# Performance work log

Hardware: AMD Instinct MI355X
Metric: run time of the kernel (lower is better)

## Reference

```python
import jax, jax.numpy as jnp
import numpy as np

N, E = 50000, 800000
IN_DIM, HID, HEADS, OUT_DIM, EDGE_DIM = 128, 32, 4, 64, 32


def _glorot(key, shape, dtype=jnp.float32):
    fan_in, fan_out = shape[0], shape[1]
    lim = np.sqrt(6.0 / (fan_in + fan_out))
    return jax.random.uniform(key, shape, dtype, -lim, lim)


def setup_inputs() -> dict:
    key = jax.random.key(0)
    ks = jax.random.split(key, 16)
    H1 = HEADS * HID  # 128 = concat width of layer 1
    inp = {
        "x": jax.random.normal(ks[0], (N, IN_DIM), jnp.float32),
        "edge_index": jax.random.randint(ks[1], (2, E), 0, N, jnp.int64),
        "edge_feats": jax.random.normal(ks[2], (E, EDGE_DIM), jnp.float32),
        # layer 1: TransformerConv(128 -> 32, heads=4, concat=True, edge_dim=32)
        "Wq1": _glorot(ks[3], (IN_DIM, H1)), "bq1": jnp.zeros((H1,), jnp.float32),
        "Wk1": _glorot(ks[4], (IN_DIM, H1)), "bk1": jnp.zeros((H1,), jnp.float32),
        "Wv1": _glorot(ks[5], (IN_DIM, H1)), "bv1": jnp.zeros((H1,), jnp.float32),
        "We1": _glorot(ks[6], (EDGE_DIM, H1)),
        "Ws1": _glorot(ks[7], (IN_DIM, H1)), "bs1": jnp.zeros((H1,), jnp.float32),
        # layer 2: TransformerConv(128 -> 64, heads=1, concat=False, edge_dim=32)
        "Wq2": _glorot(ks[8], (H1, OUT_DIM)), "bq2": jnp.zeros((OUT_DIM,), jnp.float32),
        "Wk2": _glorot(ks[9], (H1, OUT_DIM)), "bk2": jnp.zeros((OUT_DIM,), jnp.float32),
        "Wv2": _glorot(ks[10], (H1, OUT_DIM)), "bv2": jnp.zeros((OUT_DIM,), jnp.float32),
        "We2": _glorot(ks[11], (EDGE_DIM, OUT_DIM)),
        "Ws2": _glorot(ks[12], (H1, OUT_DIM)), "bs2": jnp.zeros((OUT_DIM,), jnp.float32),
    }
    return inp


def _tconv(x, src, dst, e, Wq, bq, Wk, bk, Wv, bv, We, Ws, bs, heads, concat):
    """PyG TransformerConv: gather q_i/k_j/v_j, add edge embedding to k and v,
    segment-softmax over incoming edges of each target node, scatter-aggregate."""
    n = x.shape[0]
    d = Wq.shape[1] // heads
    q = (x @ Wq + bq).reshape(n, heads, d)
    k = (x @ Wk + bk).reshape(n, heads, d)
    v = (x @ Wv + bv).reshape(n, heads, d)
    ee = (e @ We).reshape(-1, heads, d)      # [E, H, D]
    kj = k[src] + ee                          # [E, H, D]
    vj = v[src] + ee                          # [E, H, D]
    a = jnp.einsum('ehd,ehd->eh', q[dst], kj) / jnp.sqrt(jnp.asarray(d, x.dtype))
    amax = jax.ops.segment_max(a, dst, num_segments=n)      # [N, H]
    ex = jnp.exp(a - amax[dst])
    den = jax.ops.segment_sum(ex, dst, num_segments=n)
    alpha = ex / den[dst]                                   # [E, H]
    out = jax.ops.segment_sum(alpha[..., None] * vj, dst, num_segments=n)
    out = out.reshape(n, heads * d) if concat else out.mean(axis=1)
    return out + x @ Ws + bs  # root/skip connection (lin_skip)


def reference(x, edge_index, edge_feats,
              Wq1, bq1, Wk1, bk1, Wv1, bv1, We1, Ws1, bs1,
              Wq2, bq2, Wk2, bk2, Wv2, bv2, We2, Ws2, bs2):
    src, dst = edge_index[0], edge_index[1]  # flow='source_to_target'
    h = _tconv(x, src, dst, edge_feats, Wq1, bq1, Wk1, bk1, Wv1, bv1,
               We1, Ws1, bs1, heads=HEADS, concat=True)
    h = jax.nn.relu(h)  # activation; dropout p=0.0 is identity
    h = _tconv(h, src, dst, edge_feats, Wq2, bq2, Wk2, bk2, Wv2, bv2,
               We2, Ws2, bs2, heads=1, concat=False)
    return h
```

## Files before the change

### kernel.cpp

```cpp
#include <hip/hip_runtime.h>
#include <hip/hip_bf16.h>


typedef unsigned int  u32;
typedef unsigned short u16;
typedef __attribute__((ext_vector_type(8))) __bf16 bf16x8;
typedef __attribute__((ext_vector_type(4))) float  f32x4;

#define S1L (0.17677669529663687f * 1.4426950408889634f)
#define S2L (0.125f * 1.4426950408889634f)

__device__ __forceinline__ u16 f2bf(float f) {
    u32 u = __float_as_uint(f);
    u32 r = (u + 0x7fffu + ((u >> 16) & 1u)) >> 16;
    return (u16)r;
}
__device__ __forceinline__ float bflo(u32 u) { return __uint_as_float(u << 16); }
__device__ __forceinline__ float bfhi(u32 u) { return __uint_as_float(u & 0xffff0000u); }

template<int CTRL>
__device__ __forceinline__ float dpp_add(float x) {
    int y = __builtin_amdgcn_mov_dpp(__float_as_int(x), CTRL, 0xF, 0xF, true);
    return x + __int_as_float(y);
}

__global__ void k_hist(const int* __restrict__ dst, int* __restrict__ deg, int nE) {
    int e = blockIdx.x * 256 + threadIdx.x;
    if (e < nE) atomicAdd(&deg[dst[e]], 1);
}

__global__ __launch_bounds__(1024) void k_scan_part(const int* __restrict__ deg,
                                                    int* __restrict__ rp,
                                                    int* __restrict__ csum, int nN)
{
    __shared__ int buf[1024];
    const int tid = threadIdx.x, idx = blockIdx.x * 1024 + tid;
    int v = (idx < nN) ? deg[idx] : 0;
    buf[tid] = v;
    __syncthreads();
    for (int off = 1; off < 1024; off <<= 1) {
        int t = (tid >= off) ? buf[tid - off] : 0;
        __syncthreads();
        buf[tid] += t;
        __syncthreads();
    }
    if (idx < nN) rp[idx] = buf[tid] - v;
    if (tid == 1023) csum[blockIdx.x] = buf[1023];
}

__global__ __launch_bounds__(1024) void k_scan_tot(int* __restrict__ csum, int nb,
                                                   int* __restrict__ rowptr, int nN, int nE)
{
    __shared__ int buf[1024];
    const int tid = threadIdx.x;
    int v = (tid < nb) ? csum[tid] : 0;
    buf[tid] = v;
    __syncthreads();
    for (int off = 1; off < 1024; off <<= 1) {
        int t = (tid >= off) ? buf[tid - off] : 0;
        __syncthreads();
        buf[tid] += t;
        __syncthreads();
    }
    if (tid < nb) csum[tid] = buf[tid] - v;
    if (tid == 0) rowptr[nN] = nE;
}

__global__ void k_scan_apply(int* __restrict__ rp, const int* __restrict__ csum,
                             int* __restrict__ fill, int nN)
{
    int i = blockIdx.x * 256 + threadIdx.x;
    if (i < nN) { int r = rp[i] + csum[i >> 10]; rp[i] = r; fill[i] = r; }
}

__global__ void k_scatter_prep(
    const int* __restrict__ src, const int* __restrict__ dst,
    int* __restrict__ fill, int2* __restrict__ se, int nE,
    const float* __restrict__ Wq1, const float* __restrict__ Wk1,
    const float* __restrict__ Wv1, const float* __restrict__ Ws1,
    const float* __restrict__ Wq2, const float* __restrict__ Wk2,
    const float* __restrict__ Wv2, const float* __restrict__ Ws2,
    const float* __restrict__ We1, const float* __restrict__ We2,
    const float* __restrict__ bq1, const float* __restrict__ bq2,
    u16* __restrict__ WB1, u16* __restrict__ WB2,
    float* __restrict__ bqe1, float* __restrict__ bqe2,
    const float4* __restrict__ x4, uint2* __restrict__ xb4, int nN)
{
    long g = (long)blockIdx.x * 256 + threadIdx.x;
    if (g < nE) {
        int e = (int)g;
        int p = atomicAdd(&fill[dst[e]], 1);
        se[p] = make_int2(src[e], e);
        return;
    }
    long t = g - nE;
    if (t < 65536) {
        int j = (int)t >> 7, k = (int)t & 127;
        int m = j >> 7, col = j & 127;
        const float* W = (m == 0) ? Wq1 : (m == 1) ? Wk1 : (m == 2) ? Wv1 : Ws1;
        WB1[t] = f2bf(W[k * 128 + col]);
        return;
    }
    t -= 65536;
    if (t < 49152) {
        int j = (int)t >> 7, k = (int)t & 127;
        if (j < 256) {
            int m = j >> 6, col = j & 63;
            const float* W = (m == 0) ? Wq2 : (m == 1) ? Wk2 : (m == 2) ? Wv2 : Ws2;
            WB2[t] = f2bf(W[k * 64 + col]);
        } else if (j >= 288) {
            WB2[t] = 0;
        }
        return;
    }
    t -= 49152;
    if (t < 16384) {
        int j = (int)t >> 7, m = (int)t & 127;
        int h = j >> 5, c = j & 31;
        float acc = 0.f;
        #pragma unroll
        for (int d = 0; d < 32; ++d)
            acc += Wq1[m * 128 + h * 32 + d] * We1[c * 128 + h * 32 + d];
        WB1[512 * 128 + j * 128 + m] = f2bf(acc * S1L);
        if (m == 0) {
            float b = 0.f;
            #pragma unroll
            for (int d = 0; d < 32; ++d)
                b += bq1[h * 32 + d] * We1[c * 128 + h * 32 + d];
            bqe1[j] = b * S1L;
        }
        return;
    }
    t -= 16384;
    if (t < 4096) {
        int c = (int)t >> 7, m = (int)t & 127;
        float acc = 0.f;
        #pragma unroll
        for (int d = 0; d < 64; ++d)
            acc += Wq2[m * 64 + d] * We2[c * 64 + d];
        WB2[256 * 128 + c * 128 + m] = f2bf(acc * S2L);
        if (m == 0) {
            float b = 0.f;
            #pragma unroll
            for (int d = 0; d < 64; ++d) b += bq2[d] * We2[c * 64 + d];
            bqe2[c] = b * S2L;
        }
        return;
    }
    t -= 4096;
    if (t < (long)nN * 32) {
        float4 f = x4[t];
        xb4[t] = make_uint2((u32)f2bf(f.x) | ((u32)f2bf(f.y) << 16),
                            (u32)f2bf(f.z) | ((u32)f2bf(f.w) << 16));
    }
}

__global__ void k_ef_gather(const int2* __restrict__ se, const float4* __restrict__ ef4,
                            uint2* __restrict__ efc2, int nE)
{
    int t = blockIdx.x * 256 + threadIdx.x;
    int p = t >> 3, sub = t & 7;
    if (p >= nE) return;
    int e = se[p].y;
    float4 f = ef4[(size_t)e * 8 + sub];
    efc2[(size_t)p * 8 + sub] =
        make_uint2((u32)f2bf(f.x) | ((u32)f2bf(f.y) << 16),
                   (u32)f2bf(f.z) | ((u32)f2bf(f.w) << 16));
}

__global__ __launch_bounds__(256) void k_lin_gemm1(
    const u16* __restrict__ xb, const u16* __restrict__ WB,
    const float* __restrict__ bq, const float* __restrict__ bk,
    const float* __restrict__ bv, const float* __restrict__ bs,
    const float* __restrict__ bqe,
    u32* __restrict__ qqe1, u32* __restrict__ kv1, float* __restrict__ sk1, int nN)
{
    __shared__ __align__(16) u16 lds[2 * 128 * 128];
    const int tid = threadIdx.x;
    const int ct = blockIdx.y;
    const int rowbase = blockIdx.x * 128;

    {
        const int lr = tid >> 4, kc = tid & 15;
        #pragma unroll
        for (int it = 0; it < 8; ++it) {
            int row = it * 16 + lr;
            int grow = rowbase + row; if (grow >= nN) grow = nN - 1;
            uint4 va = *(const uint4*)(xb + (size_t)grow * 128 + kc * 8);
            *(uint4*)((char*)lds + row * 256 + ((kc * 16) ^ ((row & 7) << 4))) = va;
        }
        #pragma unroll
        for (int it = 0; it < 8; ++it) {
            int row = it * 16 + lr;
            uint4 vb = *(const uint4*)(WB + ((size_t)ct * 128 + row) * 128 + kc * 8);
            *(uint4*)((char*)lds + 32768 + row * 256 + ((kc * 16) ^ ((row & 7) << 4))) = vb;
        }
    }
    __syncthreads();

    const int wave = tid >> 6, lane = tid & 63;
    const int wr = wave >> 1, wc = wave & 1;
    const int colL = lane & 15, kgrp = lane >> 4;

    f32x4 acc[4][4];
    #pragma unroll
    for (int m = 0; m < 4; ++m)
        #pragma unroll
        for (int n = 0; n < 4; ++n) acc[m][n] = {0.f, 0.f, 0.f, 0.f};

    #pragma unroll
    for (int ks = 0; ks < 4; ++ks) {
        const int kb = ks * 64 + kgrp * 16;
        bf16x8 af[4], bfr[4];
        #pragma unroll
        for (int m = 0; m < 4; ++m) {
            int row = wr * 64 + m * 16 + colL;
            af[m] = *(const bf16x8*)((const char*)lds + row * 256 + (kb ^ ((row & 7) << 4)));
        }
        #pragma unroll
        for (int n = 0; n < 4; ++n) {
            int row = wc * 64 + n * 16 + colL;
            bfr[n] = *(const bf16x8*)((const char*)lds + 32768 + row * 256 + (kb ^ ((row & 7) << 4)));
        }
        #pragma unroll
        for (int m = 0; m < 4; ++m)
            #pragma unroll
            for (int n = 0; n < 4; ++n)
                acc[m][n] = __builtin_amdgcn_mfma_f32_16x16x32_bf16(af[m], bfr[n], acc[m][n], 0, 0, 0);
    }

    const float* bias = (ct == 0) ? bq : (ct == 1) ? bk : (ct == 2) ? bv : (ct == 3) ? bs : bqe;
    const float scale = (ct == 0) ? S1L : 1.f;
    const bool  is32 = (ct == 3);
    const int   hi = (ct == 2 || ct == 4) ? 1 : 0;
    u32* dstw = (ct == 3) ? (u32*)sk1 : ((ct == 1 || ct == 2) ? kv1 : qqe1);

    #pragma unroll
    for (int n = 0; n < 4; ++n) {
        const int c = wc * 64 + n * 16 + colL;
        const float bval = bias[c];
        #pragma unroll
        for (int m = 0; m < 4; ++m) {
            #pragma unroll
            for (int i = 0; i < 4; ++i) {
                const int r = rowbase + wr * 64 + m * 16 + kgrp * 4 + i;
                if (r < nN) {
                    float v = (acc[m][n][i] + bval) * scale;
                    if (is32) ((float*)dstw)[(size_t)r * 128 + c] = v;
                    else ((u16*)dstw)[(((size_t)r * 128 + c) << 1) + hi] = f2bf(v);
                }
            }
        }
    }
}

__global__ __launch_bounds__(256) void k_lin_gemm2(
    const u16* __restrict__ hb, const u16* __restrict__ WB,
    const float* __restrict__ bq, const float* __restrict__ bk,
    const float* __restrict__ bv, const float* __restrict__ bs,
    const float* __restrict__ bqe,
    float* __restrict__ q2, u32* __restrict__ kv2, float* __restrict__ sk2,
    float* __restrict__ qe2, int nN)
{
    __shared__ __align__(16) u16 lds[2 * 128 * 128];
    const int tid = threadIdx.x;
    const int ct = blockIdx.y;
    const int rowbase = blockIdx.x * 128;

    {
        const int lr = tid >> 4, kc = tid & 15;
        #pragma unroll
        for (int it = 0; it < 8; ++it) {
            int row = it * 16 + lr;
            int grow = rowbase + row; if (grow >= nN) grow = nN - 1;
            uint4 va = *(const uint4*)(hb + (size_t)grow * 128 + kc * 8);
            *(uint4*)((char*)lds + row * 256 + ((kc * 16) ^ ((row & 7) << 4))) = va;
        }
        #pragma unroll
        for (int it = 0; it < 8; ++it) {
            int row = it * 16 + lr;
            uint4 vb = *(const uint4*)(WB + ((size_t)ct * 128 + row) * 128 + kc * 8);
            *(uint4*)((char*)lds + 32768 + row * 256 + ((kc * 16) ^ ((row & 7) << 4))) = vb;
        }
    }
    __syncthreads();

    const int wave = tid >> 6, lane = tid & 63;
    const int wr = wave >> 1, wc = wave & 1;
    const int colL = lane & 15, kgrp = lane >> 4;

    f32x4 acc[4][4];
    #pragma unroll
    for (int m = 0; m < 4; ++m)
        #pragma unroll
        for (int n = 0; n < 4; ++n) acc[m][n] = {0.f, 0.f, 0.f, 0.f};

    #pragma unroll
    for (int ks = 0; ks < 4; ++ks) {
        const int kb = ks * 64 + kgrp * 16;
        bf16x8 af[4], bfr[4];
        #pragma unroll
        for (int m = 0; m < 4; ++m) {
            int row = wr * 64 + m * 16 + colL;
            af[m] = *(const bf16x8*)((const char*)lds + row * 256 + (kb ^ ((row & 7) << 4)));
        }
        #pragma unroll
        for (int n = 0; n < 4; ++n) {
            int row = wc * 64 + n * 16 + colL;
            bfr[n] = *(const bf16x8*)((const char*)lds + 32768 + row * 256 + (kb ^ ((row & 7) << 4)));
        }
        #pragma unroll
        for (int m = 0; m < 4; ++m)
            #pragma unroll
            for (int n = 0; n < 4; ++n)
                acc[m][n] = __builtin_amdgcn_mfma_f32_16x16x32_bf16(af[m], bfr[n], acc[m][n], 0, 0, 0);
    }

    const int mode = ct * 2 + wc;
    if (mode == 5) return;

    #pragma unroll
    for (int n = 0; n < 4; ++n) {
        const int cl = n * 16 + colL;
        float bval;
        if (mode == 0) bval = bq[cl];
        else if (mode == 1) bval = bk[cl];
        else if (mode == 2) bval = bv[cl];
        else if (mode == 3) bval = bs[cl];
        else bval = (cl < 32) ? bqe[cl] : 0.f;
        #pragma unroll
        for (int m = 0; m < 4; ++m) {
            #pragma unroll
            for (int i = 0; i < 4; ++i) {
                const int r = rowbase + wr * 64 + m * 16 + kgrp * 4 + i;
                if (r < nN) {
                    const float v = acc[m][n][i] + bval;
                    if (mode == 0)      q2[(size_t)r * 64 + cl] = v * S2L;
                    else if (mode == 1) ((u16*)kv2)[(((size_t)r * 64 + cl) << 1)] = f2bf(v);
                    else if (mode == 2) ((u16*)kv2)[(((size_t)r * 64 + cl) << 1) + 1] = f2bf(v);
                    else if (mode == 3) sk2[(size_t)r * 64 + cl] = v;
                    else if (cl < 32)   qe2[(size_t)r * 32 + cl] = v;
                }
            }
        }
    }
}

__global__ __launch_bounds__(256) void k_agg1f(
    const int* __restrict__ rowptr, const int2* __restrict__ se,
    const u16* __restrict__ efc, const u32* __restrict__ qqe1,
    const u32* __restrict__ kv1, const float* __restrict__ sk1,
    const float* __restrict__ We, u16* __restrict__ h1b, int nN, int stride4)
{
    __shared__ float lsv[4][128];
    __shared__ float lsef[4][128];
    __shared__ float lden[4][4];
    const int wave = threadIdx.x >> 6, lane = threadIdx.x & 63;
    const int es = lane >> 5;
    const int h  = (lane >> 3) & 3;
    const int c8 = lane & 7;
    const int jb = h * 32 + c8 * 4;
    const int jA = lane, jB = lane + 64;
    const int hA = jA >> 5, hB = jB >> 5;
    float wA[32], wB[32];
    #pragma unroll
    for (int c = 0; c < 32; ++c) {
        wA[c] = We[c * 128 + jA];
        wB[c] = We[c * 128 + jB];
    }

    for (int dbase = blockIdx.x * 4; dbase < nN; dbase += stride4) {
        const int d = dbase + wave;
        const bool act = d < nN;
        float den = 0.f;
        float4 sv = {0.f, 0.f, 0.f, 0.f}, sef = sv;
        if (act) {
            const uint4 qq = *(const uint4*)(qqe1 + (size_t)d * 128 + jb);
            const float4 qr  = {bflo(qq.x), bflo(qq.y), bflo(qq.z), bflo(qq.w)};
            const float4 qer = {bfhi(qq.x), bfhi(qq.y), bfhi(qq.z), bfhi(qq.w)};
            const int beg = rowptr[d], end = rowptr[d + 1];
            for (int cbeg = beg; cbeg < end; cbeg += 64) {
                const int cnt = min(64, end - cbeg);
                const int sreg = se[cbeg + (lane < cnt ? lane : cnt - 1)].x;
                #pragma unroll 2
                for (int t = 0; t < cnt; t += 2) {
                    const int idx = t + es;
                    const bool valid = idx < cnt;
                    const int s = __shfl(sreg, idx);
                    const int iec = cbeg + (valid ? idx : 0);
                    const uint4 kp = *(const uint4*)(kv1 + ((u32)s << 7) + jb);
                    const uint2 ee = *(const uint2*)(efc + ((size_t)iec << 5) + c8 * 4);
                    const float f0 = bflo(ee.x), f1 = bfhi(ee.x);
                    const float f2 = bflo(ee.y), f3 = bfhi(ee.y);
                    float p = qr.x * bflo(kp.x) + qr.y * bflo(kp.y)
                            + qr.z * bflo(kp.z) + qr.w * bflo(kp.w)
                            + qer.x * f0 + qer.y * f1 + qer.z * f2 + qer.w * f3;
                    p = dpp_add<0xB1>(p);
                    p = dpp_add<0x4E>(p);
                    p = dpp_add<0x141>(p);
                    const float ex = valid ? exp2f(p) : 0.f;
                    den += ex;
                    sv.x += ex * bfhi(kp.x); sv.y += ex * bfhi(kp.y);
                    sv.z += ex * bfhi(kp.z); sv.w += ex * bfhi(kp.w);
                    sef.x += ex * f0; sef.y += ex * f1; sef.z += ex * f2; sef.w += ex * f3;
                }
            }
            den  += __shfl_xor(den, 32);
            sv.x += __shfl_xor(sv.x, 32); sv.y += __shfl_xor(sv.y, 32);
            sv.z += __shfl_xor(sv.z, 32); sv.w += __shfl_xor(sv.w, 32);
            sef.x += __shfl_xor(sef.x, 32); sef.y += __shfl_xor(sef.y, 32);
            sef.z += __shfl_xor(sef.z, 32); sef.w += __shfl_xor(sef.w, 32);
            if (es == 0) {
                *(float4*)&lsv[wave][jb]  = sv;
                *(float4*)&lsef[wave][jb] = sef;
                if (c8 == 0) lden[wave][h] = den;
            }
        }
        __syncthreads();
        if (act) {
            const float ddA = lden[wave][hA], ddB = lden[wave][hB];
            const float invA = ddA > 0.f ? 1.0f / ddA : 0.f;
            const float invB = ddB > 0.f ? 1.0f / ddB : 0.f;
            float aA = lsv[wave][jA], aB = lsv[wave][jB];
            const float* spA = &lsef[wave][hA * 32];
            const float* spB = &lsef[wave][hB * 32];
            #pragma unroll
            for (int c = 0; c < 32; ++c) {
                aA = fmaf(spA[c], wA[c], aA);
                aB = fmaf(spB[c], wB[c], aB);
            }
            float oA = aA * invA + sk1[(size_t)d * 128 + jA];
            float oB = aB * invB + sk1[(size_t)d * 128 + jB];
            h1b[(size_t)d * 128 + jA] = f2bf(oA > 0.f ? oA : 0.f);
            h1b[(size_t)d * 128 + jB] = f2bf(oB > 0.f ? oB : 0.f);
        }
        __syncthreads();
    }
}

__global__ __launch_bounds__(256) void k_agg2f(
    const int* __restrict__ rowptr, const int2* __restrict__ se,
    const u16* __restrict__ efc, const float* __restrict__ q2,
    const float* __restrict__ qe2, const u32* __restrict__ kv2,
    const float* __restrict__ sk2, const float* __restrict__ We,
    float* __restrict__ out, int nN, int stride4)
{
    __shared__ float lsv[4][64];
    __shared__ float lsef[4][32];
    __shared__ float lden[4];
    const int wave = threadIdx.x >> 6, lane = threadIdx.x & 63;
    const int es  = lane >> 4;
    const int c16 = lane & 15;
    const int jb  = c16 * 4;
    const int ce  = (c16 & 7) * 4;
    float wreg[32];
    #pragma unroll
    for (int c = 0; c < 32; ++c) wreg[c] = We[c * 64 + lane];

    for (int dbase = blockIdx.x * 4; dbase < nN; dbase += stride4) {
        const int d = dbase + wave;
        const bool act = d < nN;
        float den = 0.f;
        float4 sv = {0.f, 0.f, 0.f, 0.f}, sef = sv;
        if (act) {
            const float4 qr = *(const float4*)(q2 + (size_t)d * 64 + jb);
            float4 qer = {0.f, 0.f, 0.f, 0.f};
            if (c16 < 8) qer = *(const float4*)(qe2 + (size_t)d * 32 + jb);
            const int beg = rowptr[d], end = rowptr[d + 1];
            for (int cbeg = beg; cbeg < end; cbeg += 64) {
                const int cnt = min(64, end - cbeg);
                const int sreg = se[cbeg + (lane < cnt ? lane : cnt - 1)].x;
                #pragma unroll 2
                for (int t = 0; t < cnt; t += 4) {
                    const int idx = t + es;
                    const bool valid = idx < cnt;
                    const int s = __shfl(sreg, idx);
                    const int iec = cbeg + (valid ? idx : 0);
                    const uint4 kp = *(const uint4*)(kv2 + ((u32)s << 6) + jb);
                    const uint2 ee = *(const uint2*)(efc + ((size_t)iec << 5) + ce);
                    const float f0 = bflo(ee.x), f1 = bfhi(ee.x);
                    const float f2 = bflo(ee.y), f3 = bfhi(ee.y);
                    float p = qr.x * bflo(kp.x) + qr.y * bflo(kp.y)
                            + qr.z * bflo(kp.z) + qr.w * bflo(kp.w)
                            + qer.x * f0 + qer.y * f1 + qer.z * f2 + qer.w * f3;
                    p = dpp_add<0xB1>(p);
                    p = dpp_add<0x4E>(p);
                    p = dpp_add<0x141>(p);
                    p = dpp_add<0x140>(p);
                    const float ex = valid ? exp2f(p) : 0.f;
                    den += ex;
                    sv.x += ex * bfhi(kp.x); sv.y += ex * bfhi(kp.y);
                    sv.z += ex * bfhi(kp.z); sv.w += ex * bfhi(kp.w);
                    sef.x += ex * f0; sef.y += ex * f1; sef.z += ex * f2; sef.w += ex * f3;
                }
            }
            #pragma unroll
            for (int m = 16; m <= 32; m <<= 1) {
                den  += __shfl_xor(den, m);
                sv.x += __shfl_xor(sv.x, m); sv.y += __shfl_xor(sv.y, m);
                sv.z += __shfl_xor(sv.z, m); sv.w += __shfl_xor(sv.w, m);
                sef.x += __shfl_xor(sef.x, m); sef.y += __shfl_xor(sef.y, m);
                sef.z += __shfl_xor(sef.z, m); sef.w += __shfl_xor(sef.w, m);
            }
            if (es == 0) {
                *(float4*)&lsv[wave][jb] = sv;
                if (c16 < 8) *(float4*)&lsef[wave][jb] = sef;
                if (c16 == 0) lden[wave] = den;
            }
        }
        __syncthreads();
        if (act) {
            const float dd = lden[wave];
            const float inv = dd > 0.f ? 1.0f / dd : 0.f;
            float a = lsv[wave][lane];
            #pragma unroll
            for (int c = 0; c < 32; ++c) a = fmaf(lsef[wave][c], wreg[c], a);
            out[(size_t)d * 64 + lane] = a * inv + sk2[(size_t)d * 64 + lane];
        }
        __syncthreads();
    }
}

extern "C" void kernel_launch(void* const* d_in, const int* in_sizes, int n_in,
                              void* d_out, int out_size, void* d_ws, size_t ws_size,
                              hipStream_t stream)
{
    const float* x   = (const float*)d_in[0];
    const int*   ei  = (const int*)d_in[1];
    const float* ef  = (const float*)d_in[2];
    const float* Wq1 = (const float*)d_in[3];  const float* bq1 = (const float*)d_in[4];
    const float* Wk1 = (const float*)d_in[5];  const float* bk1 = (const float*)d_in[6];
    const float* Wv1 = (const float*)d_in[7];  const float* bv1 = (const float*)d_in[8];
    const float* We1 = (const float*)d_in[9];
    const float* Ws1 = (const float*)d_in[10]; const float* bs1 = (const float*)d_in[11];
    const float* Wq2 = (const float*)d_in[12]; const float* bq2 = (const float*)d_in[13];
    const float* Wk2 = (const float*)d_in[14]; const float* bk2 = (const float*)d_in[15];
    const float* Wv2 = (const float*)d_in[16]; const float* bv2 = (const float*)d_in[17];
    const float* We2 = (const float*)d_in[18];
    const float* Ws2 = (const float*)d_in[19]; const float* bs2 = (const float*)d_in[20];

    const int nN = in_sizes[0] / 128;
    const int nE = in_sizes[1] / 2;
    const int* srcv = ei;
    const int* dstv = ei + nE;

    float* ws = (float*)d_ws;
    size_t off = 0;
    auto alloc = [&](size_t n) { float* p = ws + off; off += n; return p; };
    u32*   qqe1  = (u32*)alloc((size_t)nN * 128);
    float* sk1   = alloc((size_t)nN * 128);
    u32*   kv1   = (u32*)alloc((size_t)nN * 128);
    u16*   h1b   = (u16*)alloc((size_t)nN * 64);
    u16*   xb    = (u16*)alloc((size_t)nN * 64);
    u16*   efc   = (u16*)alloc((size_t)nE * 16);
    u16*   WB1   = (u16*)alloc(640 * 128 / 2);
    u16*   WB2   = (u16*)alloc(384 * 128 / 2);
    float* bqe1  = alloc(128);
    float* bqe2  = alloc(32);
    int* deg     = (int*)alloc(nN);
    int* rowptr  = (int*)alloc(nN + 1);
    int* fill    = (int*)alloc(nN);
    int* csum    = (int*)alloc(1024);
    int2* se     = (int2*)alloc((size_t)nE * 2);
    float* l2 = (float*)qqe1;
    size_t o2 = 0;
    auto alloc2 = [&](size_t n) { float* p = l2 + o2; o2 += n; return p; };
    float* q2   = alloc2((size_t)nN * 64);
    u32*   kv2  = (u32*)alloc2((size_t)nN * 64);
    (void)alloc2(0);
    float* sk2  = alloc((size_t)nN * 64);
    float* qe2  = alloc((size_t)nN * 32);
    (void)ws_size; (void)n_in; (void)out_size;

    const int nChunk = (nN + 1023) / 1024;
    const int rowTiles = (nN + 127) / 128;
    const int aggBlocks = 2048;

    hipMemsetAsync(deg, 0, (size_t)nN * sizeof(int), stream);
    k_hist<<<(nE + 255) / 256, 256, 0, stream>>>(dstv, deg, nE);
    k_scan_part<<<nChunk, 1024, 0, stream>>>(deg, rowptr, csum, nN);
    k_scan_tot<<<1, 1024, 0, stream>>>(csum, nChunk, rowptr, nN, nE);
    k_scan_apply<<<(nN + 255) / 256, 256, 0, stream>>>(rowptr, csum, fill, nN);

    long prepTotal = 65536L + 49152 + 16384 + 4096 + (long)nN * 32;
    long spTotal = (long)nE + prepTotal;
    k_scatter_prep<<<(int)((spTotal + 255) / 256), 256, 0, stream>>>(
        srcv, dstv, fill, se, nE,
        Wq1, Wk1, Wv1, Ws1, Wq2, Wk2, Wv2, Ws2, We1, We2, bq1, bq2,
        WB1, WB2, bqe1, bqe2, (const float4*)x, (uint2*)xb, nN);
    k_ef_gather<<<(nE * 8 + 255) / 256, 256, 0, stream>>>(
        se, (const float4*)ef, (uint2*)efc, nE);

    k_lin_gemm1<<<dim3(rowTiles, 5), 256, 0, stream>>>(
        xb, WB1, bq1, bk1, bv1, bs1, bqe1, qqe1, kv1, sk1, nN);
    k_agg1f<<<aggBlocks, 256, 0, stream>>>(
        rowptr, se, efc, qqe1, kv1, sk1, We1, h1b, nN, aggBlocks * 4);

    k_lin_gemm2<<<dim3(rowTiles, 3), 256, 0, stream>>>(
        h1b, WB2, bq2, bk2, bv2, bs2, bqe2, q2, kv2, sk2, qe2, nN);
    k_agg2f<<<aggBlocks, 256, 0, stream>>>(
        rowptr, se, efc, q2, qe2, kv2, sk2, We2, (float*)d_out, nN, aggBlocks * 4);
}
```

Before: 402.2 us.

## Stage edge weights in LDS and replace block barriers with wave barriers in aggregation

Both aggregation kernels now copy the edge-projection weight matrix into shared memory once per block, where each lane previously held 32 or 64 weight values in registers. This lowers register pressure and may allow more waves per SIMD. Each wave handles its own destination node and uses only its own shared-memory slices, so the block-wide __syncthreads are swapped for wave barriers and out-of-range waves simply skip. The trade is extra LDS traffic in the epilogue FMA loop and a larger shared-memory footprint per block.

```diff
diff --git a/kernel.cpp b/kernel.cpp
--- a/kernel.cpp
+++ b/kernel.cpp
@@ -352,29 +352,29 @@
     const u32* __restrict__ kv1, const float* __restrict__ sk1,
     const float* __restrict__ We, u16* __restrict__ h1b, int nN, int stride4)
 {
+    __shared__ float Wes[32 * 128];
     __shared__ float lsv[4][128];
     __shared__ float lsef[4][128];
     __shared__ float lden[4][4];
-    const int wave = threadIdx.x >> 6, lane = threadIdx.x & 63;
+    const int tid = threadIdx.x;
+    for (int i = tid; i < 1024; i += 256)
+        ((float4*)Wes)[i] = ((const float4*)We)[i];
+    __syncthreads();
+
+    const int wave = tid >> 6, lane = tid & 63;
     const int es = lane >> 5;
     const int h  = (lane >> 3) & 3;
     const int c8 = lane & 7;
     const int jb = h * 32 + c8 * 4;
     const int jA = lane, jB = lane + 64;
     const int hA = jA >> 5, hB = jB >> 5;
-    float wA[32], wB[32];
-    #pragma unroll
-    for (int c = 0; c < 32; ++c) {
-        wA[c] = We[c * 128 + jA];
-        wB[c] = We[c * 128 + jB];
-    }
 
     for (int dbase = blockIdx.x * 4; dbase < nN; dbase += stride4) {
         const int d = dbase + wave;
-        const bool act = d < nN;
+        if (d >= nN) continue;
         float den = 0.f;
         float4 sv = {0.f, 0.f, 0.f, 0.f}, sef = sv;
-        if (act) {
+        {
             const uint4 qq = *(const uint4*)(qqe1 + (size_t)d * 128 + jb);
             const float4 qr  = {bflo(qq.x), bflo(qq.y), bflo(qq.z), bflo(qq.w)};
             const float4 qer = {bfhi(qq.x), bfhi(qq.y), bfhi(qq.z), bfhi(qq.w)};
@@ -416,8 +416,8 @@
                 if (c8 == 0) lden[wave][h] = den;
             }
         }
-        __syncthreads();
-        if (act) {
+        __builtin_amdgcn_wave_barrier();
+        {
             const float ddA = lden[wave][hA], ddB = lden[wave][hB];
             const float invA = ddA > 0.f ? 1.0f / ddA : 0.f;
             const float invB = ddB > 0.f ? 1.0f / ddB : 0.f;
@@ -426,15 +426,15 @@
             const float* spB = &lsef[wave][hB * 32];
             #pragma unroll
             for (int c = 0; c < 32; ++c) {
-                aA = fmaf(spA[c], wA[c], aA);
-                aB = fmaf(spB[c], wB[c], aB);
+                aA = fmaf(spA[c], Wes[c * 128 + jA], aA);
+                aB = fmaf(spB[c], Wes[c * 128 + jB], aB);
             }
             float oA = aA * invA + sk1[(size_t)d * 128 + jA];
             float oB = aB * invB + sk1[(size_t)d * 128 + jB];
             h1b[(size_t)d * 128 + jA] = f2bf(oA > 0.f ? oA : 0.f);
             h1b[(size_t)d * 128 + jB] = f2bf(oB > 0.f ? oB : 0.f);
         }
-        __syncthreads();
+        __builtin_amdgcn_wave_barrier();
     }
 }
 
@@ -445,24 +445,27 @@
     const float* __restrict__ sk2, const float* __restrict__ We,
     float* __restrict__ out, int nN, int stride4)
 {
+    __shared__ float Wes[32 * 64];
     __shared__ float lsv[4][64];
     __shared__ float lsef[4][32];
     __shared__ float lden[4];
-    const int wave = threadIdx.x >> 6, lane = threadIdx.x & 63;
+    const int tid = threadIdx.x;
+    for (int i = tid; i < 512; i += 256)
+        ((float4*)Wes)[i] = ((const float4*)We)[i];
+    __syncthreads();
+
+    const int wave = tid >> 6, lane = tid & 63;
     const int es  = lane >> 4;
     const int c16 = lane & 15;
     const int jb  = c16 * 4;
     const int ce  = (c16 & 7) * 4;
-    float wreg[32];
-    #pragma unroll
-    for (int c = 0; c < 32; ++c) wreg[c] = We[c * 64 + lane];
 
     for (int dbase = blockIdx.x * 4; dbase < nN; dbase += stride4) {
         const int d = dbase + wave;
-        const bool act = d < nN;
+        if (d >= nN) continue;
         float den = 0.f;
         float4 sv = {0.f, 0.f, 0.f, 0.f}, sef = sv;
-        if (act) {
+        {
             const float4 qr = *(const float4*)(q2 + (size_t)d * 64 + jb);
             float4 qer = {0.f, 0.f, 0.f, 0.f};
             if (c16 < 8) qer = *(const float4*)(qe2 + (size_t)d * 32 + jb);
@@ -508,16 +511,16 @@
                 if (c16 == 0) lden[wave] = den;
             }
         }
-        __syncthreads();
-        if (act) {
+        __builtin_amdgcn_wave_barrier();
+        {
             const float dd = lden[wave];
             const float inv = dd > 0.f ? 1.0f / dd : 0.f;
             float a = lsv[wave][lane];
             #pragma unroll
-            for (int c = 0; c < 32; ++c) a = fmaf(lsef[wave][c], wreg[c], a);
+            for (int c = 0; c < 32; ++c) a = fmaf(lsef[wave][c], Wes[c * 64 + lane], a);
             out[(size_t)d * 64 + lane] = a * inv + sk2[(size_t)d * 64 + lane];
         }
-        __syncthreads();
+        __builtin_amdgcn_wave_barrier();
     }
 }
 
@@ -567,7 +570,6 @@
     auto alloc2 = [&](size_t n) { float* p = l2 + o2; o2 += n; return p; };
     float* q2   = alloc2((size_t)nN * 64);
     u32*   kv2  = (u32*)alloc2((size_t)nN * 64);
-    (void)alloc2(0);
     float* sk2  = alloc((size_t)nN * 64);
     float* qe2  = alloc((size_t)nN * 32);
     (void)ws_size; (void)n_in; (void)out_size;
```

Measured after the change: 389.1 us. 1.03x faster.
